# Optimization experiments

Measured on AMD Instinct MI355X. Metric: run time of the kernel, lower is better.

Reference implementation:

```python
import jax, jax.numpy as jnp
import numpy as np

NUM_TAGS = 3


def setup_inputs() -> dict:
    key = jax.random.key(0)
    k1, k2, k3 = jax.random.split(key, 3)
    B, T, K = 2048, 4096, NUM_TAGS
    logits = jax.random.normal(k1, (B, T, K), dtype=jnp.float32)
    transitions = jax.random.normal(k2, (K, K), dtype=jnp.float32)
    tags = jax.random.randint(k3, (B, T), 0, K, dtype=jnp.int64)
    return {"logits": logits, "transitions": transitions, "tags": tags}


def reference(logits, transitions, tags):
    """Negative CRF log-likelihood (AllenNLP CRF, include_start_end_transitions=False,
    full mask), i.e. -(sum_b [joint_score(b) - log_partition(b)])."""
    # --- log partition via forward algorithm (lax.scan over time) ---
    # alpha: [B, K]; emissions scanned over time: [T-1, B, K]
    def step(alpha, emit_t):
        # broadcast: alpha[b, i] + transitions[i, j] -> logsumexp over i
        new_alpha = jax.nn.logsumexp(alpha[:, :, None] + transitions[None, :, :], axis=1) + emit_t
        return new_alpha, None

    alpha0 = logits[:, 0, :]                              # [B, K]
    emits_rest = jnp.swapaxes(logits[:, 1:, :], 0, 1)     # [T-1, B, K]
    alpha_T, _ = jax.lax.scan(step, alpha0, emits_rest)
    log_z = jax.nn.logsumexp(alpha_T, axis=1)             # [B]

    # --- joint (numerator) score of the gold tag sequence ---
    emit_score = jnp.take_along_axis(logits, tags[:, :, None], axis=2)[..., 0].sum(axis=1)  # [B]
    trans_score = transitions[tags[:, :-1], tags[:, 1:]].sum(axis=1)                         # [B]

    loglik = emit_score + trans_score - log_z
    return -jnp.sum(loglik)
```

## Files before the change

### kernel.cpp

```cpp
#include <hip/hip_runtime.h>

#define BB 2048
#define TT 4096
#define LN2 0.69314718055994530942f

__global__ __launch_bounds__(256, 4) void crf_pass1(
    const float* __restrict__ logits, const float* __restrict__ trans,
    const int* __restrict__ tags, float* __restrict__ ws)
{
    __shared__ float sTrans[9];
    __shared__ float sTrExp[9];
    __shared__ float sRec[3][12];
    const int tid = threadIdx.x;
    if (tid < 9) {
        float tv = trans[tid];
        sTrans[tid] = tv;
        sTrExp[tid] = __expf(tv);
    }
    __syncthreads();

    const int b = blockIdx.x;
    const int c = tid;

    float t00 = sTrExp[0], t01 = sTrExp[1], t02 = sTrExp[2];
    float t10 = sTrExp[3], t11 = sTrExp[4], t12 = sTrExp[5];
    float t20 = sTrExp[6], t21 = sTrExp[7], t22 = sTrExp[8];

    float a00 = 1.f, a01 = 0.f, a02 = 0.f;
    float a10 = 0.f, a11 = 1.f, a12 = 0.f;
    float a20 = 0.f, a21 = 0.f, a22 = 1.f;
    int   se = 0;
    float score = 0.f;
    unsigned long long acc = 0ull;
    int firstTag = 0, prev = 0;
    float v0 = 0.f, v1 = 0.f, v2 = 0.f;

    const float4* lp = (const float4*)(logits + ((size_t)b * TT + (size_t)c * 16) * 3);
    const int4*   tp = (const int4*)(tags + (size_t)b * TT + (size_t)c * 16);

    float Lf[48];
    int   Ti[16];
#pragma unroll
    for (int i = 0; i < 12; ++i) {
        float4 t = lp[i];
        Lf[4*i+0] = t.x; Lf[4*i+1] = t.y; Lf[4*i+2] = t.z; Lf[4*i+3] = t.w;
    }
#pragma unroll
    for (int i = 0; i < 4; ++i) {
        int4 t = tp[i];
        Ti[4*i+0] = t.x; Ti[4*i+1] = t.y; Ti[4*i+2] = t.z; Ti[4*i+3] = t.w;
    }
    __builtin_amdgcn_sched_barrier(0);

#define MATSTEP(e0_, e1_, e2_) do {                                     \
    float x0 = __expf(e0_), x1 = __expf(e1_), x2 = __expf(e2_);         \
    float b0 = (a00*t00 + a01*t10 + a02*t20) * x0;                      \
    float b1 = (a00*t01 + a01*t11 + a02*t21) * x1;                      \
    float b2 = (a00*t02 + a01*t12 + a02*t22) * x2;                      \
    float b3 = (a10*t00 + a11*t10 + a12*t20) * x0;                      \
    float b4 = (a10*t01 + a11*t11 + a12*t21) * x1;                      \
    float b5 = (a10*t02 + a11*t12 + a12*t22) * x2;                      \
    float b6 = (a20*t00 + a21*t10 + a22*t20) * x0;                      \
    float b7 = (a20*t01 + a21*t11 + a22*t21) * x1;                      \
    float b8 = (a20*t02 + a21*t12 + a22*t22) * x2;                      \
    a00=b0; a01=b1; a02=b2; a10=b3; a11=b4; a12=b5; a20=b6; a21=b7; a22=b8; \
} while (0)

#define RENORM9(q00,q01,q02,q10,q11,q12,q20,q21,q22) do {               \
    float m_ = fmaxf(fmaxf(fmaxf(q00, q01), fmaxf(q02, q10)),           \
                     fmaxf(fmaxf(q11, q12), fmaxf(fmaxf(q20, q21), q22))); \
    int ef_ = (int)(__float_as_uint(m_) >> 23);                         \
    float scf_ = __uint_as_float((unsigned)(254 - ef_) << 23);          \
    se += ef_ - 127;                                                    \
    q00 *= scf_; q01 *= scf_; q02 *= scf_;                              \
    q10 *= scf_; q11 *= scf_; q12 *= scf_;                              \
    q20 *= scf_; q21 *= scf_; q22 *= scf_;                              \
} while (0)

#pragma unroll
    for (int s = 0; s < 16; ++s) {
        float e0 = Lf[3*s+0], e1 = Lf[3*s+1], e2 = Lf[3*s+2];
        int tg = Ti[s];
        if (s == 0) {
            if (c == 0) {
                v0 = __expf(e0); v1 = __expf(e1); v2 = __expf(e2);
            } else {
                MATSTEP(e0, e1, e2);
            }
            firstTag = tg;
        } else {
            MATSTEP(e0, e1, e2);
            acc += 1ull << (7 * (prev * 3 + tg));
        }
        score += (tg == 0) ? e0 : ((tg == 1) ? e1 : e2);
        prev = tg;
        if ((s & 7) == 7) RENORM9(a00,a01,a02,a10,a11,a12,a20,a21,a22);
    }

#pragma unroll
    for (int p = 0; p < 9; ++p)
        score += (float)((int)((acc >> (7 * p)) & 127ull)) * sTrans[p];

    const int lane = tid & 63;
#pragma unroll
    for (int m = 1; m < 64; m <<= 1) {
        float o00 = __shfl_xor(a00, m, 64), o01 = __shfl_xor(a01, m, 64), o02 = __shfl_xor(a02, m, 64);
        float o10 = __shfl_xor(a10, m, 64), o11 = __shfl_xor(a11, m, 64), o12 = __shfl_xor(a12, m, 64);
        float o20 = __shfl_xor(a20, m, 64), o21 = __shfl_xor(a21, m, 64), o22 = __shfl_xor(a22, m, 64);
        int   osh = __shfl_xor(se, m, 64);
        float osc = __shfl_xor(score, m, 64);
        int   ofi = __shfl_xor(firstTag, m, 64);
        int   ola = __shfl_xor(prev, m, 64);
        bool low = (lane & m) == 0;
        float l00 = low ? a00 : o00, l01 = low ? a01 : o01, l02 = low ? a02 : o02;
        float l10 = low ? a10 : o10, l11 = low ? a11 : o11, l12 = low ? a12 : o12;
        float l20 = low ? a20 : o20, l21 = low ? a21 : o21, l22 = low ? a22 : o22;
        float r00 = low ? o00 : a00, r01 = low ? o01 : a01, r02 = low ? o02 : a02;
        float r10 = low ? o10 : a10, r11 = low ? o11 : a11, r12 = low ? o12 : a12;
        float r20 = low ? o20 : a20, r21 = low ? o21 : a21, r22 = low ? o22 : a22;

        float c00 = l00*r00 + l01*r10 + l02*r20;
        float c01 = l00*r01 + l01*r11 + l02*r21;
        float c02 = l00*r02 + l01*r12 + l02*r22;
        float c10 = l10*r00 + l11*r10 + l12*r20;
        float c11 = l10*r01 + l11*r11 + l12*r21;
        float c12 = l10*r02 + l11*r12 + l12*r22;
        float c20 = l20*r00 + l21*r10 + l22*r20;
        float c21 = l20*r01 + l21*r11 + l22*r21;
        float c22 = l20*r02 + l21*r12 + l22*r22;

        int Ll = low ? prev : ola;
        int Rf = low ? ofi : firstTag;
        score = score + osc + sTrans[Ll * 3 + Rf];
        se += osh;
        firstTag = low ? firstTag : ofi;
        prev = low ? ola : prev;

        a00=c00; a01=c01; a02=c02; a10=c10; a11=c11; a12=c12; a20=c20; a21=c21; a22=c22;
        RENORM9(a00,a01,a02,a10,a11,a12,a20,a21,a22);
    }

    const int wid = tid >> 6;
    if (lane == 0 && wid > 0) {
        sRec[wid-1][0] = a00; sRec[wid-1][1] = a01; sRec[wid-1][2] = a02;
        sRec[wid-1][3] = a10; sRec[wid-1][4] = a11; sRec[wid-1][5] = a12;
        sRec[wid-1][6] = a20; sRec[wid-1][7] = a21; sRec[wid-1][8] = a22;
        sRec[wid-1][9]  = __int_as_float(se);
        sRec[wid-1][10] = score;
        sRec[wid-1][11] = __int_as_float(firstTag | (prev << 8));
    }
    __syncthreads();
    if (tid == 0) {
#pragma unroll
        for (int k = 0; k < 3; ++k) {
            float m00 = sRec[k][0], m01 = sRec[k][1], m02 = sRec[k][2];
            float m10 = sRec[k][3], m11 = sRec[k][4], m12 = sRec[k][5];
            float m20 = sRec[k][6], m21 = sRec[k][7], m22 = sRec[k][8];
            int   shm = __float_as_int(sRec[k][9]);
            float scm = sRec[k][10];
            int   pkm = __float_as_int(sRec[k][11]);

            float c00 = a00*m00 + a01*m10 + a02*m20;
            float c01 = a00*m01 + a01*m11 + a02*m21;
            float c02 = a00*m02 + a01*m12 + a02*m22;
            float c10 = a10*m00 + a11*m10 + a12*m20;
            float c11 = a10*m01 + a11*m11 + a12*m21;
            float c12 = a10*m02 + a11*m12 + a12*m22;
            float c20 = a20*m00 + a21*m10 + a22*m20;
            float c21 = a20*m01 + a21*m11 + a22*m21;
            float c22 = a20*m02 + a21*m12 + a22*m22;

            score += scm + sTrans[prev * 3 + (pkm & 255)];
            prev = pkm >> 8;
            se += shm;
            a00=c00; a01=c01; a02=c02; a10=c10; a11=c11; a12=c12; a20=c20; a21=c21; a22=c22;
            RENORM9(a00,a01,a02,a10,a11,a12,a20,a21,a22);
        }
        float n0 = v0*a00 + v1*a10 + v2*a20;
        float n1 = v0*a01 + v1*a11 + v2*a21;
        float n2 = v0*a02 + v1*a12 + v2*a22;
        float logz = logf(n0 + n1 + n2) + (float)se * LN2;
        ws[b] = logz - score;
    }

#undef MATSTEP
#undef RENORM9
}

__global__ __launch_bounds__(256) void crf_reduce(
    const float* __restrict__ ws, float* __restrict__ out)
{
    int tid = threadIdx.x;
    float s = 0.f;
#pragma unroll
    for (int k = 0; k < BB / 256; ++k) s += ws[k * 256 + tid];
    for (int off = 32; off > 0; off >>= 1) s += __shfl_down(s, off, 64);
    __shared__ float sP[4];
    if ((tid & 63) == 0) sP[tid >> 6] = s;
    __syncthreads();
    if (tid == 0) out[0] = sP[0] + sP[1] + sP[2] + sP[3];
}

extern "C" void kernel_launch(void* const* d_in, const int* in_sizes, int n_in,
                              void* d_out, int out_size, void* d_ws, size_t ws_size,
                              hipStream_t stream) {
    const float* logits = (const float*)d_in[0];
    const float* trans  = (const float*)d_in[1];
    const int*   tags   = (const int*)d_in[2];
    float* out = (float*)d_out;
    float* ws  = (float*)d_ws;

    crf_pass1<<<dim3(BB), dim3(256), 0, stream>>>(logits, trans, tags, ws);
    crf_reduce<<<dim3(1), dim3(256), 0, stream>>>(ws, out);
}
```

Baseline: 31.46 us.

## Pack tags into bits, use shfl_down tree scan, raise occupancy target

Register pressure is cut in several ways. The 16 tags become 2-bit fields in one word instead of an int array, the butterfly xor-shuffle with low/high selects becomes a shfl_down reduction where lane 0 ends up holding the ordered product, and the first-step emission values are reloaded from global memory only by thread 0. The occupancy hint in launch bounds goes from 4 to 5 blocks per SIMD to hide memory latency. Risks are the narrower register budget causing spills and shfl_down reading out-of-range lanes, which is harmless because only lane 0 is used.

```diff
diff --git a/kernel.cpp b/kernel.cpp
--- a/kernel.cpp
+++ b/kernel.cpp
@@ -4,7 +4,7 @@
 #define TT 4096
 #define LN2 0.69314718055994530942f
 
-__global__ __launch_bounds__(256, 4) void crf_pass1(
+__global__ __launch_bounds__(256, 5) void crf_pass1(
     const float* __restrict__ logits, const float* __restrict__ trans,
     const int* __restrict__ tags, float* __restrict__ ws)
 {
@@ -22,6 +22,27 @@
     const int b = blockIdx.x;
     const int c = tid;
 
+    const int4*   tp = (const int4*)(tags + (size_t)b * TT + (size_t)c * 16);
+    const float4* lp = (const float4*)(logits + ((size_t)b * TT + (size_t)c * 16) * 3);
+
+    int4 Tq[4];
+#pragma unroll
+    for (int i = 0; i < 4; ++i) Tq[i] = tp[i];
+    float Lf[48];
+#pragma unroll
+    for (int i = 0; i < 12; ++i) {
+        float4 t = lp[i];
+        Lf[4*i+0] = t.x; Lf[4*i+1] = t.y; Lf[4*i+2] = t.z; Lf[4*i+3] = t.w;
+    }
+    __builtin_amdgcn_sched_barrier(0);
+
+    unsigned pk = 0;
+#pragma unroll
+    for (int i = 0; i < 4; ++i) {
+        pk |= ((unsigned)Tq[i].x << (8*i))     | ((unsigned)Tq[i].y << (8*i+2))
+            | ((unsigned)Tq[i].z << (8*i+4))   | ((unsigned)Tq[i].w << (8*i+6));
+    }
+
     float t00 = sTrExp[0], t01 = sTrExp[1], t02 = sTrExp[2];
     float t10 = sTrExp[3], t11 = sTrExp[4], t12 = sTrExp[5];
     float t20 = sTrExp[6], t21 = sTrExp[7], t22 = sTrExp[8];
@@ -32,25 +53,7 @@
     int   se = 0;
     float score = 0.f;
     unsigned long long acc = 0ull;
-    int firstTag = 0, prev = 0;
-    float v0 = 0.f, v1 = 0.f, v2 = 0.f;
-
-    const float4* lp = (const float4*)(logits + ((size_t)b * TT + (size_t)c * 16) * 3);
-    const int4*   tp = (const int4*)(tags + (size_t)b * TT + (size_t)c * 16);
-
-    float Lf[48];
-    int   Ti[16];
-#pragma unroll
-    for (int i = 0; i < 12; ++i) {
-        float4 t = lp[i];
-        Lf[4*i+0] = t.x; Lf[4*i+1] = t.y; Lf[4*i+2] = t.z; Lf[4*i+3] = t.w;
-    }
-#pragma unroll
-    for (int i = 0; i < 4; ++i) {
-        int4 t = tp[i];
-        Ti[4*i+0] = t.x; Ti[4*i+1] = t.y; Ti[4*i+2] = t.z; Ti[4*i+3] = t.w;
-    }
-    __builtin_amdgcn_sched_barrier(0);
+    int prev = 0;
 
 #define MATSTEP(e0_, e1_, e2_) do {                                     \
     float x0 = __expf(e0_), x1 = __expf(e1_), x2 = __expf(e2_);         \
@@ -66,81 +69,68 @@
     a00=b0; a01=b1; a02=b2; a10=b3; a11=b4; a12=b5; a20=b6; a21=b7; a22=b8; \
 } while (0)
 
-#define RENORM9(q00,q01,q02,q10,q11,q12,q20,q21,q22) do {               \
-    float m_ = fmaxf(fmaxf(fmaxf(q00, q01), fmaxf(q02, q10)),           \
-                     fmaxf(fmaxf(q11, q12), fmaxf(fmaxf(q20, q21), q22))); \
+#define RENORM do {                                                     \
+    float m_ = fmaxf(fmaxf(fmaxf(a00, a01), fmaxf(a02, a10)),           \
+                     fmaxf(fmaxf(a11, a12), fmaxf(fmaxf(a20, a21), a22))); \
     int ef_ = (int)(__float_as_uint(m_) >> 23);                         \
     float scf_ = __uint_as_float((unsigned)(254 - ef_) << 23);          \
     se += ef_ - 127;                                                    \
-    q00 *= scf_; q01 *= scf_; q02 *= scf_;                              \
-    q10 *= scf_; q11 *= scf_; q12 *= scf_;                              \
-    q20 *= scf_; q21 *= scf_; q22 *= scf_;                              \
+    a00 *= scf_; a01 *= scf_; a02 *= scf_;                              \
+    a10 *= scf_; a11 *= scf_; a12 *= scf_;                              \
+    a20 *= scf_; a21 *= scf_; a22 *= scf_;                              \
 } while (0)
 
 #pragma unroll
     for (int s = 0; s < 16; ++s) {
         float e0 = Lf[3*s+0], e1 = Lf[3*s+1], e2 = Lf[3*s+2];
-        int tg = Ti[s];
+        int tg = (int)((pk >> (2*s)) & 3u);
         if (s == 0) {
-            if (c == 0) {
-                v0 = __expf(e0); v1 = __expf(e1); v2 = __expf(e2);
-            } else {
-                MATSTEP(e0, e1, e2);
-            }
-            firstTag = tg;
+            if (c != 0) MATSTEP(e0, e1, e2);
         } else {
             MATSTEP(e0, e1, e2);
             acc += 1ull << (7 * (prev * 3 + tg));
         }
         score += (tg == 0) ? e0 : ((tg == 1) ? e1 : e2);
         prev = tg;
-        if ((s & 7) == 7) RENORM9(a00,a01,a02,a10,a11,a12,a20,a21,a22);
-    }
+        if ((s & 7) == 7) RENORM;
+    }
+
+    int firstTag = (int)(pk & 3u);
 
 #pragma unroll
     for (int p = 0; p < 9; ++p)
         score += (float)((int)((acc >> (7 * p)) & 127ull)) * sTrans[p];
 
+#pragma unroll
+    for (int m = 1; m < 64; m <<= 1) {
+        float o00 = __shfl_down(a00, m, 64), o01 = __shfl_down(a01, m, 64), o02 = __shfl_down(a02, m, 64);
+        float o10 = __shfl_down(a10, m, 64), o11 = __shfl_down(a11, m, 64), o12 = __shfl_down(a12, m, 64);
+        float o20 = __shfl_down(a20, m, 64), o21 = __shfl_down(a21, m, 64), o22 = __shfl_down(a22, m, 64);
+        int   ose = __shfl_down(se, m, 64);
+        float osc = __shfl_down(score, m, 64);
+        int   ofi = __shfl_down(firstTag, m, 64);
+        int   opv = __shfl_down(prev, m, 64);
+
+        float c00 = a00*o00 + a01*o10 + a02*o20;
+        float c01 = a00*o01 + a01*o11 + a02*o21;
+        float c02 = a00*o02 + a01*o12 + a02*o22;
+        float c10 = a10*o00 + a11*o10 + a12*o20;
+        float c11 = a10*o01 + a11*o11 + a12*o21;
+        float c12 = a10*o02 + a11*o12 + a12*o22;
+        float c20 = a20*o00 + a21*o10 + a22*o20;
+        float c21 = a20*o01 + a21*o11 + a22*o21;
+        float c22 = a20*o02 + a21*o12 + a22*o22;
+
+        score = score + osc + sTrans[prev * 3 + ofi];
+        prev = opv;
+        se += ose;
+
+        a00=c00; a01=c01; a02=c02; a10=c10; a11=c11; a12=c12; a20=c20; a21=c21; a22=c22;
+        RENORM;
+    }
+
     const int lane = tid & 63;
-#pragma unroll
-    for (int m = 1; m < 64; m <<= 1) {
-        float o00 = __shfl_xor(a00, m, 64), o01 = __shfl_xor(a01, m, 64), o02 = __shfl_xor(a02, m, 64);
-        float o10 = __shfl_xor(a10, m, 64), o11 = __shfl_xor(a11, m, 64), o12 = __shfl_xor(a12, m, 64);
-        float o20 = __shfl_xor(a20, m, 64), o21 = __shfl_xor(a21, m, 64), o22 = __shfl_xor(a22, m, 64);
-        int   osh = __shfl_xor(se, m, 64);
-        float osc = __shfl_xor(score, m, 64);
-        int   ofi = __shfl_xor(firstTag, m, 64);
-        int   ola = __shfl_xor(prev, m, 64);
-        bool low = (lane & m) == 0;
-        float l00 = low ? a00 : o00, l01 = low ? a01 : o01, l02 = low ? a02 : o02;
-        float l10 = low ? a10 : o10, l11 = low ? a11 : o11, l12 = low ? a12 : o12;
-        float l20 = low ? a20 : o20, l21 = low ? a21 : o21, l22 = low ? a22 : o22;
-        float r00 = low ? o00 : a00, r01 = low ? o01 : a01, r02 = low ? o02 : a02;
-        float r10 = low ? o10 : a10, r11 = low ? o11 : a11, r12 = low ? o12 : a12;
-        float r20 = low ? o20 : a20, r21 = low ? o21 : a21, r22 = low ? o22 : a22;
-
-        float c00 = l00*r00 + l01*r10 + l02*r20;
-        float c01 = l00*r01 + l01*r11 + l02*r21;
-        float c02 = l00*r02 + l01*r12 + l02*r22;
-        float c10 = l10*r00 + l11*r10 + l12*r20;
-        float c11 = l10*r01 + l11*r11 + l12*r21;
-        float c12 = l10*r02 + l11*r12 + l12*r22;
-        float c20 = l20*r00 + l21*r10 + l22*r20;
-        float c21 = l20*r01 + l21*r11 + l22*r21;
-        float c22 = l20*r02 + l21*r12 + l22*r22;
-
-        int Ll = low ? prev : ola;
-        int Rf = low ? ofi : firstTag;
-        score = score + osc + sTrans[Ll * 3 + Rf];
-        se += osh;
-        firstTag = low ? firstTag : ofi;
-        prev = low ? ola : prev;
-
-        a00=c00; a01=c01; a02=c02; a10=c10; a11=c11; a12=c12; a20=c20; a21=c21; a22=c22;
-        RENORM9(a00,a01,a02,a10,a11,a12,a20,a21,a22);
-    }
-
-    const int wid = tid >> 6;
+    const int wid  = tid >> 6;
     if (lane == 0 && wid > 0) {
         sRec[wid-1][0] = a00; sRec[wid-1][1] = a01; sRec[wid-1][2] = a02;
         sRec[wid-1][3] = a10; sRec[wid-1][4] = a11; sRec[wid-1][5] = a12;
@@ -174,8 +164,12 @@
             prev = pkm >> 8;
             se += shm;
             a00=c00; a01=c01; a02=c02; a10=c10; a11=c11; a12=c12; a20=c20; a21=c21; a22=c22;
-            RENORM9(a00,a01,a02,a10,a11,a12,a20,a21,a22);
+            RENORM;
         }
+        const float* lb = logits + (size_t)b * TT * 3;
+        float v0 = __expf(lb[0]);
+        float v1 = __expf(lb[1]);
+        float v2 = __expf(lb[2]);
         float n0 = v0*a00 + v1*a10 + v2*a20;
         float n1 = v0*a01 + v1*a11 + v2*a21;
         float n2 = v0*a02 + v1*a12 + v2*a22;
@@ -184,7 +178,7 @@
     }
 
 #undef MATSTEP
-#undef RENORM9
+#undef RENORM
 }
 
 __global__ __launch_bounds__(256) void crf_reduce(
```

Result: slower. 32.86 us (+4.5%).
